# Performance work log

Hardware: AMD Instinct MI355X
Metric: run time of the kernel (lower is better)

## Reference

```python
import jax, jax.numpy as jnp
import numpy as np

# pywt db4 decomposition filters (dec_lo, dec_hi), 8 taps
DEC_LO = np.array([-0.010597401784997278, 0.032883011666982945, 0.030841381835986965,
                   -0.18703481171888114, -0.02798376941698385, 0.6308807679295904,
                   0.7148465705525415, 0.23037781330885523])
DEC_HI = np.array([-0.23037781330885523, 0.7148465705525415, -0.6308807679295904,
                   -0.02798376941698385, 0.18703481171888114, 0.030841381835986965,
                   -0.032883011666982945, -0.010597401784997278])
HEADS = 8


def dwt_db4(v):
    # Equivalent of pywt.dwt(v, 'db4') (mode='symmetric') applied along last axis.
    # Symmetric (half-point) extension by L-1=7, full convolution, downsample taking
    # every 2nd sample starting at conv index 1 -> out_len = floor((n+7)/2).
    pad = [(0, 0)] * (v.ndim - 1) + [(7, 7)]
    ext = jnp.pad(v, pad, mode='symmetric')[..., 1:]
    lead = v.shape[:-1]
    lhs = ext.reshape(-1, 1, ext.shape[-1])                       # (N, 1, n+13)
    rhs = jnp.stack([jnp.asarray(DEC_LO[::-1], v.dtype),
                     jnp.asarray(DEC_HI[::-1], v.dtype)])[:, None, :]  # (2, 1, 8)
    out = jax.lax.conv_general_dilated(lhs, rhs, (2,), 'VALID')   # (N, 2, out_len)
    out = out.reshape(*lead, 2, -1)
    return out[..., 0, :], out[..., 1, :]


def setup_inputs() -> dict:
    key = jax.random.key(0)
    k0, k1, k2, k3 = jax.random.split(key, 4)
    B, S, H = 4, 2048, 1024
    a = float(np.sqrt(6.0 / (H + H)))  # xavier_uniform bound
    x = jax.random.normal(k0, (B, S, H), dtype=jnp.float32)
    Wq = jax.random.uniform(k1, (H, H), jnp.float32, -a, a)
    Wk = jax.random.uniform(k2, (H, H), jnp.float32, -a, a)
    Wv = jax.random.uniform(k3, (H, H), jnp.float32, -a, a)
    return {"x": x, "Wq": Wq, "Wk": Wk, "Wv": Wv}


def reference(x, Wq, Wk, Wv):
    B, S, Hd = x.shape
    H = HEADS
    dk = Hd // H
    scale = dk ** -0.5
    # torch nn.Linear: y = x @ W.T
    q = (x @ Wq.T).reshape(B, S, H, dk).transpose(0, 2, 1, 3) * scale  # (B,H,S,dk)
    k = (x @ Wk.T).reshape(B, S, H, dk).transpose(0, 2, 1, 3)
    v = (x @ Wv.T).reshape(B, S, H, dk).transpose(0, 2, 1, 3)
    attn = jax.nn.softmax(jnp.einsum('bhqd,bhkd->bhqk', q, k), axis=-1)
    cA, cD = dwt_db4(v)                                   # (B,H,S,wA) each
    wA = cA.shape[-1]
    wcD = jnp.einsum('bhqk,bhkw->bhqw', attn, cD)
    out1 = wcD.transpose(0, 2, 1, 3).reshape(B, S, H * wA)
    out2 = cA.reshape(-1, S, H * wA)                      # faithful raw view of (B,H,S,wA)
    return out1, out2
```

## Files before the change

### kernel.cpp

```cpp
#include <hip/hip_runtime.h>
#include <hip/hip_bf16.h>

#define B_ 4
#define S_ 2048
#define HD 1024
#define NH 8
#define DK 128
#define WA 67
#define WPAD 80

typedef __attribute__((ext_vector_type(8))) short short8;
typedef __attribute__((ext_vector_type(4))) short short4v;
typedef __attribute__((ext_vector_type(4))) float floatx4;

__device__ __forceinline__ float hexp2(float x) { return __builtin_amdgcn_exp2f(x); }

__device__ __forceinline__ short f2bf(float f) {
    union { float f; unsigned u; } c; c.f = f;
    unsigned u = c.u;
    u += 0x7FFF + ((u >> 16) & 1);
    return (short)(u >> 16);
}
__device__ __forceinline__ float bf2f(short s) {
    union { unsigned u; float f; } c; c.u = ((unsigned)(unsigned short)s) << 16;
    return c.f;
}
__device__ __forceinline__ short f2bf_trunc(float f) {
    union { float f; unsigned u; } c; c.f = f;
    return (short)(c.u >> 16);
}

__device__ __forceinline__ void glds16(void* lds, const void* g) {
    __builtin_amdgcn_global_load_lds(
        (const __attribute__((address_space(1))) unsigned*)g,
        (__attribute__((address_space(3))) unsigned*)lds, 16, 0, 0);
}

__device__ __constant__ float FLO[8] = {
    0.23037781330885523f,  0.7148465705525415f,  0.6308807679295904f,
   -0.02798376941698385f, -0.18703481171888114f, 0.030841381835986965f,
    0.032883011666982945f, -0.010597401784997278f };
__device__ __constant__ float FHI[8] = {
   -0.010597401784997278f, -0.032883011666982945f, 0.030841381835986965f,
    0.18703481171888114f,  -0.02798376941698385f, -0.6308807679295904f,
    0.7148465705525415f,   -0.23037781330885523f };

__global__ __launch_bounds__(256) void cvt_all(
    const float* __restrict__ x,  const float* __restrict__ wq,
    const float* __restrict__ wk, const float* __restrict__ wv,
    short* __restrict__ xb, short* __restrict__ wb)
{
    const size_t w_elems = (size_t)HD * HD;
    int blk = blockIdx.x;
    const float* src; short* dst; int lb;
    if (blk < 4096)      { src = x;  dst = xb;               lb = blk; }
    else if (blk < 4608) { src = wq; dst = wb;               lb = blk - 4096; }
    else if (blk < 5120) { src = wk; dst = wb + w_elems;     lb = blk - 4608; }
    else                 { src = wv; dst = wb + 2 * w_elems; lb = blk - 5120; }
    int i = lb * 256 + threadIdx.x;
    const float4* s = (const float4*)src + (size_t)i * 2;
    float4 f0 = s[0], f1 = s[1];
    short8 o;
    o[0] = f2bf(f0.x); o[1] = f2bf(f0.y); o[2] = f2bf(f0.z); o[3] = f2bf(f0.w);
    o[4] = f2bf(f1.x); o[5] = f2bf(f1.y); o[6] = f2bf(f1.z); o[7] = f2bf(f1.w);
    *((short8*)dst + i) = o;
}

__global__ __launch_bounds__(256, 2) void qkv_gemm(
    const short* __restrict__ xb, const short* __restrict__ Wb,
    short* __restrict__ Qb, short* __restrict__ Kb,
    float* __restrict__ outA, short* __restrict__ cdt)
{
    __shared__ __align__(16) short SM[32768];
    const int tid  = threadIdx.x;
    const int wid  = tid >> 6;
    const int lane = tid & 63;
    const int l15  = lane & 15;
    const int quad = lane >> 4;
    const int rx   = l15 & 7;
    const int wm   = wid >> 1;
    const int wn   = wid & 1;
    const int m0 = blockIdx.x * 128;
    const int by = blockIdx.y;
    const int z  = by >> 3;
    const int n0 = (by & 7) * 128;
    const short* W = Wb + (size_t)z * HD * HD;
    const float scale = (z == 0) ? 0.12751743786072596f : 1.0f;
    const int srow = lane >> 3;
    const int sch  = (lane & 7) ^ srow;

    floatx4 acc[4][4] = {};

    auto Abuf = [&](int bf) -> short* { return SM + bf * 8192; };
    auto Bbuf = [&](int bf) -> short* { return SM + 16384 + bf * 8192; };

    auto stA = [&](int bf, int t) {
        short* d = Abuf(bf);
        #pragma unroll
        for (int i = 0; i < 4; ++i) {
            int ti = wid * 4 + i;
            glds16(d + ti * 512,
                   xb + (size_t)(m0 + ti * 8 + srow) * HD + t * 64 + sch * 8);
        }
    };
    auto stB = [&](int bf, int t) {
        short* d = Bbuf(bf);
        #pragma unroll
        for (int i = 0; i < 4; ++i) {
            int ti = wid * 4 + i;
            glds16(d + ti * 512,
                   W + (size_t)(n0 + ti * 8 + srow) * HD + t * 64 + sch * 8);
        }
    };

#define VM0 asm volatile("s_waitcnt vmcnt(0)" ::: "memory")
#define BARRIER do { asm volatile("" ::: "memory"); \
                     __builtin_amdgcn_s_barrier(); \
                     asm volatile("" ::: "memory"); } while (0)

    stA(0, 0); stB(0, 0);
    VM0; BARRIER;

    for (int t = 0; t < 16; ++t) {
        const int cur = t & 1, nxt = cur ^ 1;
        if (t < 15) { stA(nxt, t + 1); stB(nxt, t + 1); }
        const short* Ab = Abuf(cur);
        const short* Bb = Bbuf(cur);
        #pragma unroll
        for (int ks = 0; ks < 2; ++ks) {
            short8 af[4], bf4[4];
            #pragma unroll
            for (int mt = 0; mt < 4; ++mt)
                af[mt] = *(const short8*)
                    &Ab[(wm * 64 + mt * 16 + l15) * 64 + (((ks * 4 + quad) ^ rx) * 8)];
            #pragma unroll
            for (int nt = 0; nt < 4; ++nt)
                bf4[nt] = *(const short8*)
                    &Bb[(wn * 64 + nt * 16 + l15) * 64 + (((ks * 4 + quad) ^ rx) * 8)];
            __builtin_amdgcn_s_setprio(1);
            #pragma unroll
            for (int mt = 0; mt < 4; ++mt)
                #pragma unroll
                for (int nt = 0; nt < 4; ++nt)
                    acc[mt][nt] = __builtin_amdgcn_mfma_f32_16x16x32_bf16(
                        af[mt], bf4[nt], acc[mt][nt], 0, 0, 0);
            __builtin_amdgcn_s_setprio(0);
        }
        VM0;
        BARRIER;
    }

    if (z != 2) {
        short* Yb = (z == 0) ? Qb : Kb;
        #pragma unroll
        for (int mt = 0; mt < 4; ++mt)
            #pragma unroll
            for (int nt = 0; nt < 4; ++nt)
                #pragma unroll
                for (int reg = 0; reg < 4; ++reg) {
                    int rg = m0 + wm * 64 + mt * 16 + quad * 4 + reg;
                    int cg = n0 + wn * 64 + nt * 16 + l15;
                    int b = rg >> 11, s = rg & 2047;
                    int h = cg >> 7,  d = cg & 127;
                    Yb[((size_t)(b * NH + h) * S_ + s) * DK + d] =
                        f2bf(acc[mt][nt][reg] * scale);
                }
        return;
    }
    short* Cs = SM;
    #pragma unroll
    for (int mt = 0; mt < 4; ++mt)
        #pragma unroll
        for (int nt = 0; nt < 4; ++nt)
            #pragma unroll
            for (int reg = 0; reg < 4; ++reg) {
                int r = wm * 64 + mt * 16 + quad * 4 + reg;
                int c = wn * 64 + nt * 16 + l15;
                Cs[r * 130 + c] = f2bf(acc[mt][nt][reg]);
            }
    __syncthreads();
    const int rl    = tid & 127;
    const int chunk = tid >> 7;
    const int rg = m0 + rl;
    const int b = rg >> 11, s = rg & 2047;
    const int bh = b * NH + (by & 7);
    const short* vr = Cs + rl * 130;
    auto getv = [&](int i) -> float {
        int k = (i < 6) ? (5 - i) : (i < 134) ? (i - 6) : (261 - i);
        return bf2f(vr[k]);
    };
    const int t0 = chunk * 34;
    const int t1 = (chunk == 0) ? 34 : WA;
    float win[8];
    #pragma unroll
    for (int j = 0; j < 8; ++j) win[j] = getv(2 * t0 + j);
    float* oA = outA + ((size_t)bh * S_ + s) * WA;
    for (int t = t0; t < t1; ++t) {
        float lo = 0.f, hi = 0.f;
        #pragma unroll
        for (int j = 0; j < 8; ++j) { lo += win[j] * FLO[j]; hi += win[j] * FHI[j]; }
        oA[t] = lo;
        cdt[((size_t)bh * WPAD + t) * S_ + s] = f2bf(hi);
        #pragma unroll
        for (int j = 0; j < 6; ++j) win[j] = win[j + 2];
        if (t + 1 < t1) { win[6] = getv(2 * t + 8); win[7] = getv(2 * t + 9); }
    }
    if (chunk == 1) {
        #pragma unroll
        for (int w = WA; w < WPAD; ++w)
            cdt[((size_t)bh * WPAD + w) * S_ + s] =
                (w == 67) ? (short)0x3F80 : (short)0;
    }
#undef BARRIER
#undef VM0
}

__global__ __launch_bounds__(256, 2) void attn_kernel(
    const short* __restrict__ Qb, const short* __restrict__ Kb,
    const short* __restrict__ cdt, float* __restrict__ out1)
{
    __shared__ __align__(16) short Ks[64 * 128];
    __shared__ __align__(16) short Ds[WPAD * 64];
    __shared__ __align__(16) short Pt[8 * 1024];
    const int tid  = threadIdx.x;
    const int wv   = tid >> 6;
    const int lane = tid & 63;
    const int l15  = lane & 15;
    const int quad = lane >> 4;
    const int qt = blockIdx.x;
    const int bh = blockIdx.y;
    const int b = bh >> 3, h = bh & 7;
    const int rxor = l15 & 7;

    short8 aq[2][4];
    #pragma unroll
    for (int n = 0; n < 2; ++n) {
        const short* qrow =
            Qb + ((size_t)bh * S_ + qt * 128 + wv * 32 + n * 16 + l15) * DK;
        #pragma unroll
        for (int s4 = 0; s4 < 4; ++s4)
            aq[n][s4] = *(const short8*)(qrow + s4 * 32 + quad * 8);
    }

    floatx4 O[2][5] = {};

    const short* kbase = Kb + (size_t)bh * S_ * DK;
    const int krow = lane >> 4;
    const int kch  = (lane & 15);
    const int drow = lane >> 3;
    const int dch  = (lane & 7) ^ (drow & 7);
    short* ptw = Pt + wv * 2048;

    for (int kt = 0; kt < 32; ++kt) {
        __syncthreads();
        #pragma unroll
        for (int i = 0; i < 4; ++i) {
            int ti = wv * 4 + i;
            int r  = ti * 4 + krow;
            int ch = kch ^ (r & 7);
            glds16(Ks + ti * 512, kbase + ((size_t)kt * 64 + r) * DK + ch * 8);
        }
        #pragma unroll
        for (int i = 0; i < 3; ++i) {
            int t = wv + i * 4;
            if (t < 10) {
                int r = t * 8 + drow;
                glds16(Ds + t * 512,
                       cdt + ((size_t)bh * WPAD + r) * S_ + kt * 64 + dch * 8);
            }
        }
        __syncthreads();

        floatx4 sc[2][4] = {};
        #pragma unroll
        for (int s4 = 0; s4 < 4; ++s4) {
            short8 kf[4];
            #pragma unroll
            for (int mt = 0; mt < 4; ++mt) {
                int ch = (s4 * 4 + quad) ^ rxor;
                kf[mt] = *(const short8*)&Ks[(mt * 16 + l15) * 128 + ch * 8];
            }
            #pragma unroll
            for (int n = 0; n < 2; ++n)
                #pragma unroll
                for (int mt = 0; mt < 4; ++mt)
                    sc[n][mt] = __builtin_amdgcn_mfma_f32_16x16x32_bf16(
                        kf[mt], aq[n][s4], sc[n][mt], 0, 0, 0);
        }
        #pragma unroll
        for (int n = 0; n < 2; ++n) {
            #pragma unroll
            for (int mt = 0; mt < 4; ++mt) {
                short4v pk;
                #pragma unroll
                for (int reg = 0; reg < 4; ++reg)
                    pk[reg] = f2bf_trunc(hexp2(sc[n][mt][reg]));
                int ch = (mt * 2 + (quad >> 1)) ^ rxor;
                *(short4v*)&ptw[n * 1024 + l15 * 64 + ch * 8 + (quad & 1) * 4] = pk;
            }
        }
        short8 ap[2][2];
        #pragma unroll
        for (int mt = 0; mt < 2; ++mt)
            #pragma unroll
            for (int ks = 0; ks < 2; ++ks) {
                int ch = (ks * 4 + quad) ^ rxor;
                ap[mt][ks] = *(const short8*)&ptw[mt * 1024 + l15 * 64 + ch * 8];
            }
        #pragma unroll
        for (int j = 0; j < 5; ++j) {
            #pragma unroll
            for (int ks = 0; ks < 2; ++ks) {
                int ch = (ks * 4 + quad) ^ rxor;
                short8 bd = *(const short8*)&Ds[(j * 16 + l15) * 64 + ch * 8];
                #pragma unroll
                for (int mt = 0; mt < 2; ++mt)
                    O[mt][j] = __builtin_amdgcn_mfma_f32_16x16x32_bf16(
                        ap[mt][ks], bd, O[mt][j], 0, 0, 0);
            }
        }
    }
    float rl[2][4];
    #pragma unroll
    for (int mt = 0; mt < 2; ++mt)
        #pragma unroll
        for (int reg = 0; reg < 4; ++reg)
            rl[mt][reg] = 1.0f / __shfl(O[mt][4][reg], (quad << 4) | 3, 64);
    #pragma unroll
    for (int mt = 0; mt < 2; ++mt)
        #pragma unroll
        for (int j = 0; j < 5; ++j) {
            int w = j * 16 + l15;
            if (w < WA) {
                #pragma unroll
                for (int reg = 0; reg < 4; ++reg) {
                    int qrow_g = qt * 128 + wv * 32 + mt * 16 + quad * 4 + reg;
                    out1[((size_t)(b * S_ + qrow_g)) * (NH * WA) + h * WA + w] =
                        O[mt][j][reg] * rl[mt][reg];
                }
            }
        }
}

extern "C" void kernel_launch(void* const* d_in, const int* in_sizes, int n_in,
                              void* d_out, int out_size, void* d_ws, size_t ws_size,
                              hipStream_t stream)
{
    const float* x  = (const float*)d_in[0];
    const float* Wq = (const float*)d_in[1];
    const float* Wk = (const float*)d_in[2];
    const float* Wv = (const float*)d_in[3];
    float* out = (float*)d_out;

    const size_t x_elems   = (size_t)B_ * S_ * HD;
    const size_t w_elems   = (size_t)HD * HD;
    const size_t qkv_elems = (size_t)B_ * NH * S_ * DK;
    short* xb  = (short*)d_ws;
    short* Wb  = xb + x_elems;
    short* Qb  = Wb + 3 * w_elems;
    short* Kb  = Qb + qkv_elems;
    short* cdt = Kb + qkv_elems;
    float* out1 = out;
    float* out2 = out + (size_t)B_ * S_ * NH * WA;

    cvt_all<<<dim3(5632), 256, 0, stream>>>(x, Wq, Wk, Wv, xb, Wb);
    qkv_gemm<<<dim3(64, 24), 256, 0, stream>>>(xb, Wb, Qb, Kb, out2, cdt);
    attn_kernel<<<dim3(16, 32), 256, 0, stream>>>(Qb, Kb, cdt, out1);
}
```

Measured before the change: 222.3 us.

## Double-buffer K and cD tiles in attention loop with MFMA priority hints

The attention kernel now keeps two LDS buffers for the K and transposed-cD tiles. It issues the global-to-LDS loads for the next key tile before computing on the current one, and replaces the two per-iteration syncthreads with a single vmcnt wait plus barrier at the end of each iteration. The aim is to hide global load latency behind the QK and PV MFMA work. MFMA blocks are also wrapped in s_setprio hints. The cost is double the LDS for the K and D tiles, which may reduce occupancy below the requested two blocks per CU.

```diff
diff --git a/kernel.cpp b/kernel.cpp
--- a/kernel.cpp
+++ b/kernel.cpp
@@ -35,6 +35,11 @@
         (const __attribute__((address_space(1))) unsigned*)g,
         (__attribute__((address_space(3))) unsigned*)lds, 16, 0, 0);
 }
+
+#define VM0 asm volatile("s_waitcnt vmcnt(0)" ::: "memory")
+#define BARRIER do { asm volatile("" ::: "memory"); \
+                     __builtin_amdgcn_s_barrier(); \
+                     asm volatile("" ::: "memory"); } while (0)
 
 __device__ __constant__ float FLO[8] = {
     0.23037781330885523f,  0.7148465705525415f,  0.6308807679295904f,
@@ -113,11 +118,6 @@
         }
     };
 
-#define VM0 asm volatile("s_waitcnt vmcnt(0)" ::: "memory")
-#define BARRIER do { asm volatile("" ::: "memory"); \
-                     __builtin_amdgcn_s_barrier(); \
-                     asm volatile("" ::: "memory"); } while (0)
-
     stA(0, 0); stB(0, 0);
     VM0; BARRIER;
 
@@ -211,16 +211,14 @@
             cdt[((size_t)bh * WPAD + w) * S_ + s] =
                 (w == 67) ? (short)0x3F80 : (short)0;
     }
-#undef BARRIER
-#undef VM0
 }
 
 __global__ __launch_bounds__(256, 2) void attn_kernel(
     const short* __restrict__ Qb, const short* __restrict__ Kb,
     const short* __restrict__ cdt, float* __restrict__ out1)
 {
-    __shared__ __align__(16) short Ks[64 * 128];
-    __shared__ __align__(16) short Ds[WPAD * 64];
+    __shared__ __align__(16) short Ks[2][64 * 128];
+    __shared__ __align__(16) short Ds[2][WPAD * 64];
     __shared__ __align__(16) short Pt[8 * 1024];
     const int tid  = threadIdx.x;
     const int wv   = tid >> 6;
@@ -251,25 +249,33 @@
     const int dch  = (lane & 7) ^ (drow & 7);
     short* ptw = Pt + wv * 2048;
 
-    for (int kt = 0; kt < 32; ++kt) {
-        __syncthreads();
+    auto stK = [&](int bf, int kt) {
         #pragma unroll
         for (int i = 0; i < 4; ++i) {
             int ti = wv * 4 + i;
             int r  = ti * 4 + krow;
             int ch = kch ^ (r & 7);
-            glds16(Ks + ti * 512, kbase + ((size_t)kt * 64 + r) * DK + ch * 8);
-        }
+            glds16(&Ks[bf][ti * 512], kbase + ((size_t)kt * 64 + r) * DK + ch * 8);
+        }
+    };
+    auto stD = [&](int bf, int kt) {
         #pragma unroll
         for (int i = 0; i < 3; ++i) {
             int t = wv + i * 4;
             if (t < 10) {
                 int r = t * 8 + drow;
-                glds16(Ds + t * 512,
+                glds16(&Ds[bf][t * 512],
                        cdt + ((size_t)bh * WPAD + r) * S_ + kt * 64 + dch * 8);
             }
         }
-        __syncthreads();
+    };
+
+    stK(0, 0); stD(0, 0);
+    VM0; BARRIER;
+
+    for (int kt = 0; kt < 32; ++kt) {
+        const int cur = kt & 1, nxt = cur ^ 1;
+        if (kt < 31) { stK(nxt, kt + 1); stD(nxt, kt + 1); }
 
         floatx4 sc[2][4] = {};
         #pragma unroll
@@ -278,14 +284,16 @@
             #pragma unroll
             for (int mt = 0; mt < 4; ++mt) {
                 int ch = (s4 * 4 + quad) ^ rxor;
-                kf[mt] = *(const short8*)&Ks[(mt * 16 + l15) * 128 + ch * 8];
-            }
+                kf[mt] = *(const short8*)&Ks[cur][(mt * 16 + l15) * 128 + ch * 8];
+            }
+            __builtin_amdgcn_s_setprio(1);
             #pragma unroll
             for (int n = 0; n < 2; ++n)
                 #pragma unroll
                 for (int mt = 0; mt < 4; ++mt)
                     sc[n][mt] = __builtin_amdgcn_mfma_f32_16x16x32_bf16(
                         kf[mt], aq[n][s4], sc[n][mt], 0, 0, 0);
+            __builtin_amdgcn_s_setprio(0);
         }
         #pragma unroll
         for (int n = 0; n < 2; ++n) {
@@ -312,13 +320,17 @@
             #pragma unroll
             for (int ks = 0; ks < 2; ++ks) {
                 int ch = (ks * 4 + quad) ^ rxor;
-                short8 bd = *(const short8*)&Ds[(j * 16 + l15) * 64 + ch * 8];
+                short8 bd = *(const short8*)&Ds[cur][(j * 16 + l15) * 64 + ch * 8];
+                __builtin_amdgcn_s_setprio(1);
                 #pragma unroll
                 for (int mt = 0; mt < 2; ++mt)
                     O[mt][j] = __builtin_amdgcn_mfma_f32_16x16x32_bf16(
                         ap[mt][ks], bd, O[mt][j], 0, 0, 0);
-            }
-        }
+                __builtin_amdgcn_s_setprio(0);
+            }
+        }
+        VM0;
+        BARRIER;
     }
     float rl[2][4];
     #pragma unroll
```

New measurement: 223.7 us. No clear change (+0.7%).

## Load attention K and detail operands directly from global, shrinking query tiles

Applied to the files above, without the earlier changes.

The attention kernel stops staging K and the detail coefficients in LDS behind block-wide barriers. Each wave now reads its MFMA operands straight from global memory and relies on L2/L1 for reuse. Query tiles shrink from 128 to 64 rows, giving a one-dimensional grid of 1024 blocks with a swizzled head mapping, four-block occupancy, and s_setprio around the MFMA groups. The gain is no barriers and better occupancy, at the cost of more redundant global loads per wave and less reuse of K per fetch.

```diff
diff --git a/kernel.cpp b/kernel.cpp
--- a/kernel.cpp
+++ b/kernel.cpp
@@ -35,6 +35,11 @@
         (const __attribute__((address_space(1))) unsigned*)g,
         (__attribute__((address_space(3))) unsigned*)lds, 16, 0, 0);
 }
+
+#define VM0 asm volatile("s_waitcnt vmcnt(0)" ::: "memory")
+#define BARRIER do { asm volatile("" ::: "memory"); \
+                     __builtin_amdgcn_s_barrier(); \
+                     asm volatile("" ::: "memory"); } while (0)
 
 __device__ __constant__ float FLO[8] = {
     0.23037781330885523f,  0.7148465705525415f,  0.6308807679295904f,
@@ -113,11 +118,6 @@
         }
     };
 
-#define VM0 asm volatile("s_waitcnt vmcnt(0)" ::: "memory")
-#define BARRIER do { asm volatile("" ::: "memory"); \
-                     __builtin_amdgcn_s_barrier(); \
-                     asm volatile("" ::: "memory"); } while (0)
-
     stA(0, 0); stB(0, 0);
     VM0; BARRIER;
 
@@ -211,135 +211,96 @@
             cdt[((size_t)bh * WPAD + w) * S_ + s] =
                 (w == 67) ? (short)0x3F80 : (short)0;
     }
-#undef BARRIER
-#undef VM0
-}
-
-__global__ __launch_bounds__(256, 2) void attn_kernel(
+}
+
+__global__ __launch_bounds__(256, 4) void attn_kernel(
     const short* __restrict__ Qb, const short* __restrict__ Kb,
     const short* __restrict__ cdt, float* __restrict__ out1)
 {
-    __shared__ __align__(16) short Ks[64 * 128];
-    __shared__ __align__(16) short Ds[WPAD * 64];
-    __shared__ __align__(16) short Pt[8 * 1024];
+    __shared__ __align__(16) short Pt[4 * 1024];
     const int tid  = threadIdx.x;
     const int wv   = tid >> 6;
     const int lane = tid & 63;
     const int l15  = lane & 15;
     const int quad = lane >> 4;
-    const int qt = blockIdx.x;
-    const int bh = blockIdx.y;
+    const int bid  = blockIdx.x;
+    const int j5   = bid & 31;
+    const int qt   = bid >> 5;
+    const int bh   = (j5 & 7) * 4 + (j5 >> 3);
     const int b = bh >> 3, h = bh & 7;
     const int rxor = l15 & 7;
 
-    short8 aq[2][4];
-    #pragma unroll
-    for (int n = 0; n < 2; ++n) {
-        const short* qrow =
-            Qb + ((size_t)bh * S_ + qt * 128 + wv * 32 + n * 16 + l15) * DK;
-        #pragma unroll
-        for (int s4 = 0; s4 < 4; ++s4)
-            aq[n][s4] = *(const short8*)(qrow + s4 * 32 + quad * 8);
-    }
-
-    floatx4 O[2][5] = {};
-
-    const short* kbase = Kb + (size_t)bh * S_ * DK;
-    const int krow = lane >> 4;
-    const int kch  = (lane & 15);
-    const int drow = lane >> 3;
-    const int dch  = (lane & 7) ^ (drow & 7);
-    short* ptw = Pt + wv * 2048;
+    short8 aq[4];
+    const short* qrow = Qb + ((size_t)bh * S_ + qt * 64 + wv * 16 + l15) * DK;
+    #pragma unroll
+    for (int s4 = 0; s4 < 4; ++s4)
+        aq[s4] = *(const short8*)(qrow + s4 * 32 + quad * 8);
+
+    floatx4 O[5] = {};
+
+    const short* kfb = Kb + ((size_t)bh * S_ + l15) * DK + quad * 8;
+    const short* bdb = cdt + ((size_t)bh * WPAD + l15) * S_ + quad * 8;
+
+    short* ptw = Pt + wv * 1024;
 
     for (int kt = 0; kt < 32; ++kt) {
-        __syncthreads();
-        #pragma unroll
-        for (int i = 0; i < 4; ++i) {
-            int ti = wv * 4 + i;
-            int r  = ti * 4 + krow;
-            int ch = kch ^ (r & 7);
-            glds16(Ks + ti * 512, kbase + ((size_t)kt * 64 + r) * DK + ch * 8);
-        }
-        #pragma unroll
-        for (int i = 0; i < 3; ++i) {
-            int t = wv + i * 4;
-            if (t < 10) {
-                int r = t * 8 + drow;
-                glds16(Ds + t * 512,
-                       cdt + ((size_t)bh * WPAD + r) * S_ + kt * 64 + dch * 8);
-            }
-        }
-        __syncthreads();
-
-        floatx4 sc[2][4] = {};
+        floatx4 sc[4] = {};
         #pragma unroll
         for (int s4 = 0; s4 < 4; ++s4) {
             short8 kf[4];
             #pragma unroll
-            for (int mt = 0; mt < 4; ++mt) {
-                int ch = (s4 * 4 + quad) ^ rxor;
-                kf[mt] = *(const short8*)&Ks[(mt * 16 + l15) * 128 + ch * 8];
+            for (int mt = 0; mt < 4; ++mt)
+                kf[mt] = *(const short8*)(kfb + (size_t)(kt * 64 + mt * 16) * DK
+                                              + s4 * 32);
+            __builtin_amdgcn_s_setprio(1);
+            #pragma unroll
+            for (int mt = 0; mt < 4; ++mt)
+                sc[mt] = __builtin_amdgcn_mfma_f32_16x16x32_bf16(
+                    kf[mt], aq[s4], sc[mt], 0, 0, 0);
+            __builtin_amdgcn_s_setprio(0);
+        }
+        #pragma unroll
+        for (int mt = 0; mt < 4; ++mt) {
+            short4v pk;
+            #pragma unroll
+            for (int reg = 0; reg < 4; ++reg)
+                pk[reg] = f2bf_trunc(hexp2(sc[mt][reg]));
+            int ch = (mt * 2 + (quad >> 1)) ^ rxor;
+            *(short4v*)&ptw[l15 * 64 + ch * 8 + (quad & 1) * 4] = pk;
+        }
+        short8 ap[2];
+        #pragma unroll
+        for (int ks = 0; ks < 2; ++ks)
+            ap[ks] = *(const short8*)&ptw[l15 * 64 + (((ks * 4 + quad) ^ rxor) * 8)];
+        __builtin_amdgcn_s_setprio(1);
+        #pragma unroll
+        for (int j = 0; j < 5; ++j) {
+            #pragma unroll
+            for (int ks = 0; ks < 2; ++ks) {
+                short8 bd = *(const short8*)(bdb + (size_t)(j * 16) * S_
+                                                 + kt * 64 + ks * 32);
+                O[j] = __builtin_amdgcn_mfma_f32_16x16x32_bf16(
+                    ap[ks], bd, O[j], 0, 0, 0);
             }
-            #pragma unroll
-            for (int n = 0; n < 2; ++n)
-                #pragma unroll
-                for (int mt = 0; mt < 4; ++mt)
-                    sc[n][mt] = __builtin_amdgcn_mfma_f32_16x16x32_bf16(
-                        kf[mt], aq[n][s4], sc[n][mt], 0, 0, 0);
-        }
-        #pragma unroll
-        for (int n = 0; n < 2; ++n) {
-            #pragma unroll
-            for (int mt = 0; mt < 4; ++mt) {
-                short4v pk;
-                #pragma unroll
-                for (int reg = 0; reg < 4; ++reg)
-                    pk[reg] = f2bf_trunc(hexp2(sc[n][mt][reg]));
-                int ch = (mt * 2 + (quad >> 1)) ^ rxor;
-                *(short4v*)&ptw[n * 1024 + l15 * 64 + ch * 8 + (quad & 1) * 4] = pk;
+        }
+        __builtin_amdgcn_s_setprio(0);
+    }
+    float rl[4];
+    #pragma unroll
+    for (int reg = 0; reg < 4; ++reg)
+        rl[reg] = 1.0f / __shfl(O[4][reg], (quad << 4) | 3, 64);
+    #pragma unroll
+    for (int j = 0; j < 5; ++j) {
+        int w = j * 16 + l15;
+        if (w < WA) {
+            #pragma unroll
+            for (int reg = 0; reg < 4; ++reg) {
+                int qrow_g = qt * 64 + wv * 16 + quad * 4 + reg;
+                out1[((size_t)(b * S_ + qrow_g)) * (NH * WA) + h * WA + w] =
+                    O[j][reg] * rl[reg];
             }
         }
-        short8 ap[2][2];
-        #pragma unroll
-        for (int mt = 0; mt < 2; ++mt)
-            #pragma unroll
-            for (int ks = 0; ks < 2; ++ks) {
-                int ch = (ks * 4 + quad) ^ rxor;
-                ap[mt][ks] = *(const short8*)&ptw[mt * 1024 + l15 * 64 + ch * 8];
-            }
-        #pragma unroll
-        for (int j = 0; j < 5; ++j) {
-            #pragma unroll
-            for (int ks = 0; ks < 2; ++ks) {
-                int ch = (ks * 4 + quad) ^ rxor;
-                short8 bd = *(const short8*)&Ds[(j * 16 + l15) * 64 + ch * 8];
-                #pragma unroll
-                for (int mt = 0; mt < 2; ++mt)
-                    O[mt][j] = __builtin_amdgcn_mfma_f32_16x16x32_bf16(
-                        ap[mt][ks], bd, O[mt][j], 0, 0, 0);
-            }
-        }
-    }
-    float rl[2][4];
-    #pragma unroll
-    for (int mt = 0; mt < 2; ++mt)
-        #pragma unroll
-        for (int reg = 0; reg < 4; ++reg)
-            rl[mt][reg] = 1.0f / __shfl(O[mt][4][reg], (quad << 4) | 3, 64);
-    #pragma unroll
-    for (int mt = 0; mt < 2; ++mt)
-        #pragma unroll
-        for (int j = 0; j < 5; ++j) {
-            int w = j * 16 + l15;
-            if (w < WA) {
-                #pragma unroll
-                for (int reg = 0; reg < 4; ++reg) {
-                    int qrow_g = qt * 128 + wv * 32 + mt * 16 + quad * 4 + reg;
-                    out1[((size_t)(b * S_ + qrow_g)) * (NH * WA) + h * WA + w] =
-                        O[mt][j][reg] * rl[mt][reg];
-                }
-            }
-        }
+    }
 }
 
 extern "C" void kernel_launch(void* const* d_in, const int* in_sizes, int n_in,
@@ -365,5 +326,5 @@
 
     cvt_all<<<dim3(5632), 256, 0, stream>>>(x, Wq, Wk, Wv, xb, Wb);
     qkv_gemm<<<dim3(64, 24), 256, 0, stream>>>(xb, Wb, Qb, Kb, out2, cdt);
-    attn_kernel<<<dim3(16, 32), 256, 0, stream>>>(Qb, Kb, cdt, out1);
-}
+    attn_kernel<<<dim3(1024), 256, 0, stream>>>(Qb, Kb, cdt, out1);
+}
```

Result: slower. 519.6 us (+133.8%).
